# Optimization experiments

Hardware: AMD Instinct MI355X
Metric: run time of the kernel (lower is better)

Reference implementation:

```python
import jax, jax.numpy as jnp
import numpy as np

D_MODEL = 1024
D_STATE = 16
EXPAND = 2
D_INNER = EXPAND * D_MODEL
BATCH = 8
SEQ = 2048


def _linear_init(key, fan_in, shape):
    bound = 1.0 / np.sqrt(fan_in)
    return jax.random.uniform(key, shape, jnp.float32, -bound, bound)


def setup_inputs() -> dict:
    key = jax.random.key(0)
    ks = jax.random.split(key, 9)
    x = jax.random.normal(ks[0], (BATCH, SEQ, D_MODEL), jnp.float32)
    W_in = _linear_init(ks[1], D_MODEL, (D_MODEL, 2 * D_INNER))
    b_in = _linear_init(ks[2], D_MODEL, (2 * D_INNER,))
    W_x = _linear_init(ks[3], D_INNER, (D_INNER, 2 * D_STATE))
    b_x = _linear_init(ks[4], D_INNER, (2 * D_STATE,))
    W_dt = _linear_init(ks[5], D_INNER, (D_INNER, D_INNER))
    b_dt = _linear_init(ks[6], D_INNER, (D_INNER,))
    W_out = _linear_init(ks[7], D_INNER, (D_INNER, D_MODEL))
    b_out = _linear_init(ks[8], D_INNER, (D_MODEL,))
    # A_log = log(arange(1, d_state+1)) tiled over d_inner rows
    A = jnp.tile(jnp.arange(1, D_STATE + 1, dtype=jnp.float32), (D_INNER, 1))
    A_log = jnp.log(A)
    D_param = jnp.ones((D_INNER,), jnp.float32)
    return dict(x=x, W_in=W_in, b_in=b_in, W_x=W_x, b_x=b_x, W_dt=W_dt,
                b_dt=b_dt, W_out=W_out, b_out=b_out, A_log=A_log, D_param=D_param)


def _silu(v):
    return v * jax.nn.sigmoid(v)


def reference(x, W_in, b_in, W_x, b_x, W_dt, b_dt, W_out, b_out, A_log, D_param):
    # in_proj -> split into x branch and gate z
    xz = x @ W_in + b_in                      # [B,S,2*d_inner]
    x_proj, z = jnp.split(xz, 2, axis=-1)
    u = _silu(x_proj)                          # x_conv (no conv branch)
    A = -jnp.exp(A_log)                        # [d_inner, d_state]
    x_dbl = u @ W_x + b_x                      # [B,S,2*d_state]
    Bm, Cm = jnp.split(x_dbl, 2, axis=-1)      # each [B,S,d_state]
    dt = jax.nn.softplus(u @ W_dt + b_dt)      # [B,S,d_inner]

    # selective scan: recurrence over time via lax.scan
    uT = jnp.swapaxes(u, 0, 1)                 # [S,B,d_inner]
    dtT = jnp.swapaxes(dt, 0, 1)
    BT = jnp.swapaxes(Bm, 0, 1)                # [S,B,d_state]
    CT = jnp.swapaxes(Cm, 0, 1)

    def step(h, inp):
        u_t, dt_t, B_t, C_t = inp
        dA = jnp.exp(dt_t[..., None] * A)                       # [B,d_inner,d_state]
        h = h * dA + (dt_t * u_t)[..., None] * B_t[:, None, :]  # [B,d_inner,d_state]
        y_t = jnp.einsum('bds,bs->bd', h, C_t) + D_param * u_t  # [B,d_inner]
        return h, y_t

    h0 = jnp.zeros((x.shape[0], D_INNER, D_STATE), x.dtype)
    _, yT = jax.lax.scan(step, h0, (uT, dtT, BT, CT))
    y = jnp.swapaxes(yT, 0, 1)                 # [B,S,d_inner]
    y = y * _silu(z)
    return y @ W_out + b_out                   # [B,S,d_model]
```

## Files before the change

kernel.cpp:

```cpp
#include <hip/hip_runtime.h>
#include <hip/hip_bf16.h>

typedef __hip_bfloat16 bf16;
typedef short v8s __attribute__((ext_vector_type(8)));
typedef float v4f __attribute__((ext_vector_type(4)));

#define DMODEL 1024
#define DINNER 2048
#define NSTATE 16
#define NBATCH 8
#define SEQLEN 2048
#define MROWS  (NBATCH*SEQLEN)
#define NCHUNK 32
#define CHLEN  (SEQLEN/NCHUNK)

#define SBAR() do { __builtin_amdgcn_sched_barrier(0); \
                    __builtin_amdgcn_s_barrier(); \
                    __builtin_amdgcn_sched_barrier(0); } while(0)

__device__ __forceinline__ float b2f(bf16 x){ return __bfloat162float(x); }
__device__ __forceinline__ bf16  f2b(float x){ return __float2bfloat16(x); }

__device__ __forceinline__ void gload_lds16(const bf16* g, bf16* l){
  __builtin_amdgcn_global_load_lds((const __attribute__((address_space(1))) void*)g,
                                   (__attribute__((address_space(3))) void*)l, 16, 0, 0);
}

__global__ __launch_bounds__(256) void cvt_f32_bf16(const float* __restrict__ src,
                                                    bf16* __restrict__ dst, int n4){
  const int gid = blockIdx.x*256 + threadIdx.x;
  if (gid >= n4) return;
  const float4 v = ((const float4*)src)[gid];
  union { bf16 h[4]; short4 s; } u;
  u.h[0] = f2b(v.x); u.h[1] = f2b(v.y); u.h[2] = f2b(v.z); u.h[3] = f2b(v.w);
  ((short4*)dst)[gid] = u.s;
}

__global__ __launch_bounds__(256) void transpose64(const float* __restrict__ src,
                                                   bf16* __restrict__ dst, int K, int N){
  __shared__ bf16 t[64][65];
  const int n0 = blockIdx.x*64, k0 = blockIdx.y*64;
  const int tx = threadIdx.x & 63, ty = threadIdx.x >> 6;
  for (int r = ty; r < 64; r += 4)
    t[r][tx] = f2b(src[(size_t)(k0+r)*N + n0+tx]);
  __syncthreads();
  for (int r = ty; r < 64; r += 4)
    dst[(size_t)(n0+r)*K + k0+tx] = t[tx][r];
}

__global__ __launch_bounds__(256) void padT_wx(const float* __restrict__ wx, bf16* __restrict__ wxt){
  const int gid = blockIdx.x*256 + threadIdx.x;
  const int n = gid >> 11, k = gid & 2047;
  wxt[gid] = (n < 32) ? f2b(wx[(size_t)k*32 + n]) : f2b(0.f);
}

__global__ __launch_bounds__(256) void prep_aneg(const float* __restrict__ alog, float* __restrict__ an){
  const int gid = blockIdx.x*256 + threadIdx.x;
  an[gid] = -__expf(alog[gid]);
}

template<int EPI>
__global__ __launch_bounds__(512, 2) void gemm256(
    const bf16* __restrict__ A, int lda,
    const bf16* __restrict__ Bt,
    const float* __restrict__ bias,
    void* __restrict__ Out, int ldc, int K, int nbx)
{
  extern __shared__ __align__(16) bf16 lds[];
  const int tid = threadIdx.x;
  const int lane = tid & 63, w = tid >> 6;
  const int wm = w >> 2, wn = w & 3;
  const int lr = lane & 15, lk = lane >> 4;

  const int nwg = gridDim.x;
  const int swz = (blockIdx.x & 7) * (nwg >> 3) + (blockIdx.x >> 3);
  const int nby = nwg / nbx;
  const int bx = swz / nby, by = swz % nby;
  const int m0 = by*256, n0 = bx*256;

  const int idx0 = w*64 + lane, idx1 = 512 + idx0;
  const int r0 = idx0 >> 3, r1 = idx1 >> 3;
  const int c0 = ((idx0 & 7) ^ (r0 & 7)) * 8, c1 = ((idx1 & 7) ^ (r1 & 7)) * 8;
  const size_t offA0 = (size_t)r0*lda + c0, offA1 = (size_t)r1*lda + c1;
  const size_t offB0 = (size_t)r0*K   + c0, offB1 = (size_t)r1*K   + c1;
  const int ld0 = w*512, ld1 = 4096 + w*512;

  const bf16* Abase = A  + (size_t)m0*lda;
  const bf16* Bbase = Bt + (size_t)n0*K;

  const int kb0 = (lk*16)      ^ ((lr & 7) << 4);
  const int kb1 = (64 + lk*16) ^ ((lr & 7) << 4);
  const int arow = (wm*128 + lr) * 128;
  const int brow = (wn*64  + lr) * 128;

  v4f acc[8][4];
#pragma unroll
  for (int i=0;i<8;i++)
#pragma unroll
    for (int j=0;j<4;j++) acc[i][j] = (v4f){0.f,0.f,0.f,0.f};

  auto stageTile = [&](int t){
    const bf16* ga = Abase + (size_t)t*64;
    const bf16* gbp = Bbase + (size_t)t*64;
    bf16* la = lds + (t&1)*32768;
    bf16* lb = la + 16384;
    gload_lds16(ga + offA0,                     la + ld0);
    gload_lds16(ga + offA1,                     la + ld1);
    gload_lds16(ga + offA0 + (size_t)128*lda,   la + 8192 + ld0);
    gload_lds16(ga + offA1 + (size_t)128*lda,   la + 8192 + ld1);
    gload_lds16(gbp + offB0,                    lb + ld0);
    gload_lds16(gbp + offB1,                    lb + ld1);
    gload_lds16(gbp + offB0 + (size_t)128*K,    lb + 8192 + ld0);
    gload_lds16(gbp + offB1 + (size_t)128*K,    lb + 8192 + ld1);
  };

  const int nt = K >> 6;
  stageTile(0);

  for (int t=0; t<nt; ++t){
    const char* Ab = (const char*)(lds + (t&1)*32768);
    const char* Bb = Ab + 32768;

    asm volatile("s_waitcnt vmcnt(0)" ::: "memory");
    SBAR();
    if (t+1 < nt) stageTile(t+1);

    __builtin_amdgcn_s_setprio(1);
    v8s bfr[4][2];
#pragma unroll
    for (int j=0;j<4;j++){
      bfr[j][0] = *(const v8s*)(Bb + brow + j*2048 + kb0);
      bfr[j][1] = *(const v8s*)(Bb + brow + j*2048 + kb1);
    }
#pragma unroll
    for (int q=0;q<4;q++){
      v8s aq[2][2];
#pragma unroll
      for (int i=0;i<2;i++){
        aq[i][0] = *(const v8s*)(Ab + arow + (q*2+i)*2048 + kb0);
        aq[i][1] = *(const v8s*)(Ab + arow + (q*2+i)*2048 + kb1);
      }
#pragma unroll
      for (int i=0;i<2;i++)
#pragma unroll
        for (int j=0;j<4;j++){
          acc[q*2+i][j] = __builtin_amdgcn_mfma_f32_16x16x32_bf16(aq[i][0], bfr[j][0], acc[q*2+i][j], 0,0,0);
          acc[q*2+i][j] = __builtin_amdgcn_mfma_f32_16x16x32_bf16(aq[i][1], bfr[j][1], acc[q*2+i][j], 0,0,0);
        }
    }
    __builtin_amdgcn_s_setprio(0);
  }

  float bv[4];
#pragma unroll
  for (int j=0;j<4;j++) bv[j] = bias[n0 + wn*64 + j*16 + lr];
#pragma unroll
  for (int rb=0; rb<8; rb++){
    const int gmb = m0 + wm*128 + rb*16 + lk*4;
#pragma unroll
    for (int j=0;j<4;j++){
      const int gn = n0 + wn*64 + j*16 + lr;
#pragma unroll
      for (int r=0;r<4;r++){
        float v = acc[rb][j][r] + bv[j];
        if (EPI == 0){
          v = v / (1.f + __expf(-v));
          ((bf16*)Out)[(size_t)(gmb+r)*ldc + gn] = f2b(v);
        } else if (EPI == 1){
          v = fmaxf(v, 0.f) + log1pf(__expf(-fabsf(v)));
          ((bf16*)Out)[(size_t)(gmb+r)*ldc + gn] = f2b(v);
        } else {
          ((float*)Out)[(size_t)(gmb+r)*ldc + gn] = v;
        }
      }
    }
  }
}

template<int EPI>
__global__ __launch_bounds__(256) void gemm_bt(
    const bf16* __restrict__ A, int lda,
    const bf16* __restrict__ Bt,
    const float* __restrict__ bias,
    void* __restrict__ Out, int ldc, int K)
{
  __shared__ __align__(16) bf16 Asm[2][128*64];
  __shared__ __align__(16) bf16 Bsm[2][128*64];
  const int tid = threadIdx.x;
  const int m0 = blockIdx.y*128, n0 = blockIdx.x*128;
  const int lane = tid & 63, wid = tid >> 6;
  const int wm = wid >> 1, wn = wid & 1;
  const int lr = lane & 15, lk = lane >> 4;

  v4f acc[4][4];
#pragma unroll
  for (int i=0;i<4;i++)
#pragma unroll
    for (int j=0;j<4;j++) acc[i][j] = (v4f){0.f,0.f,0.f,0.f};

  size_t aoff[4], boff[4]; int soff[4];
#pragma unroll
  for (int i=0;i<4;i++){
    const int idx = i*256 + tid;
    const int r = idx >> 3, c8 = idx & 7;
    const int c8s = c8 ^ (r & 7);
    aoff[i] = (size_t)r*lda + c8s*8;
    boff[i] = (size_t)r*K   + c8s*8;
    soff[i] = (i*256 + wid*64)*8;
  }
  const bf16* Abase = A  + (size_t)m0*lda;
  const bf16* Bbase = Bt + (size_t)n0*K;

  auto compute = [&](int buf){
#pragma unroll
    for (int kk=0;kk<2;kk++){
      v8s af[4], bfr[4];
#pragma unroll
      for (int mi=0;mi<4;mi++){
        const int row = wm*64 + mi*16 + lr;
        const int kb = (kk*64 + lk*16) ^ ((row & 7) << 4);
        af[mi] = *(const v8s*)((const char*)&Asm[buf][0] + row*128 + kb);
      }
#pragma unroll
      for (int ni=0;ni<4;ni++){
        const int row = wn*64 + ni*16 + lr;
        const int kb = (kk*64 + lk*16) ^ ((row & 7) << 4);
        bfr[ni] = *(const v8s*)((const char*)&Bsm[buf][0] + row*128 + kb);
      }
#pragma unroll
      for (int mi=0;mi<4;mi++)
#pragma unroll
        for (int ni=0;ni<4;ni++)
          acc[mi][ni] = __builtin_amdgcn_mfma_f32_16x16x32_bf16(af[mi], bfr[ni], acc[mi][ni], 0, 0, 0);
    }
  };

  const int nt = K >> 6;
#pragma unroll
  for (int i=0;i<4;i++){
    gload_lds16(Abase + aoff[i], &Asm[0][soff[i]]);
    gload_lds16(Bbase + boff[i], &Bsm[0][soff[i]]);
  }
  int cur = 0;
  for (int t=0; t<nt-1; ++t){
    __syncthreads();
    const bf16* An = Abase + (size_t)(t+1)*64;
    const bf16* Bn = Bbase + (size_t)(t+1)*64;
#pragma unroll
    for (int i=0;i<4;i++){
      gload_lds16(An + aoff[i], &Asm[cur^1][soff[i]]);
      gload_lds16(Bn + boff[i], &Bsm[cur^1][soff[i]]);
    }
    compute(cur);
    cur ^= 1;
  }
  __syncthreads();
  compute(cur);

#pragma unroll
  for (int mi=0;mi<4;mi++){
#pragma unroll
    for (int ni=0;ni<4;ni++){
      const int gn = n0 + wn*64 + ni*16 + lr;
      float bb = (gn < 32) ? bias[gn] : 0.f;
#pragma unroll
      for (int r=0;r<4;r++){
        const int gm = m0 + wm*64 + mi*16 + lk*4 + r;
        float v = acc[mi][ni][r] + bb;
        if (gn < 32) ((float*)Out)[(size_t)gm*32 + gn] = v;
      }
    }
  }
}

__global__ __launch_bounds__(256) void scan_passA(
    const bf16* __restrict__ xz, const bf16* __restrict__ dtb,
    const float* __restrict__ bc, const float* __restrict__ an,
    float* __restrict__ hC, float* __restrict__ sD)
{
  const int bx = blockIdx.x;
  const int d = (bx & 7)*256 + threadIdx.x;
  const int b = (bx >> 3) & 7;
  const int c = bx >> 6;
  float a[16], h[16];
#pragma unroll
  for (int j=0;j<16;j++){ a[j] = an[d*16+j]; h[j] = 0.f; }
  float sdt = 0.f;
  const int m0 = b*SEQLEN + c*CHLEN;
  for (int s=0;s<CHLEN;++s){
    const size_t m = (size_t)(m0 + s);
    const float uf  = b2f(xz[m*4096 + d]);
    const float dtf = b2f(dtb[m*2048 + d]);
    const float du = dtf*uf;
    sdt += dtf;
    const float4* bp = (const float4*)&bc[m*32];
    const float4 B0=bp[0],B1=bp[1],B2=bp[2],B3=bp[3];
    const float Bv[16] = {B0.x,B0.y,B0.z,B0.w,B1.x,B1.y,B1.z,B1.w,
                          B2.x,B2.y,B2.z,B2.w,B3.x,B3.y,B3.z,B3.w};
#pragma unroll
    for (int j=0;j<16;j++)
      h[j] = h[j]*__expf(dtf*a[j]) + du*Bv[j];
  }
  const size_t off = ((size_t)(c*8 + b)*2048 + d);
  float4* hp = (float4*)&hC[off*16];
  hp[0] = make_float4(h[0],h[1],h[2],h[3]);
  hp[1] = make_float4(h[4],h[5],h[6],h[7]);
  hp[2] = make_float4(h[8],h[9],h[10],h[11]);
  hp[3] = make_float4(h[12],h[13],h[14],h[15]);
  sD[off] = sdt;
}

__global__ __launch_bounds__(256) void scan_passB(
    const float* __restrict__ an, float* __restrict__ hC, const float* __restrict__ sD)
{
  const int gid = blockIdx.x*256 + threadIdx.x;
  const int d = gid & 2047, b = gid >> 11;
  float a[16], h0[16];
#pragma unroll
  for (int j=0;j<16;j++){ a[j] = an[d*16+j]; h0[j] = 0.f; }
  for (int c=0;c<NCHUNK;c++){
    const size_t off = ((size_t)(c*8 + b)*2048 + d);
    float4* hp = (float4*)&hC[off*16];
    const float4 t0=hp[0], t1=hp[1], t2=hp[2], t3=hp[3];
    const float sdt = sD[off];
    const float ht[16] = {t0.x,t0.y,t0.z,t0.w,t1.x,t1.y,t1.z,t1.w,
                          t2.x,t2.y,t2.z,t2.w,t3.x,t3.y,t3.z,t3.w};
    hp[0] = make_float4(h0[0],h0[1],h0[2],h0[3]);
    hp[1] = make_float4(h0[4],h0[5],h0[6],h0[7]);
    hp[2] = make_float4(h0[8],h0[9],h0[10],h0[11]);
    hp[3] = make_float4(h0[12],h0[13],h0[14],h0[15]);
#pragma unroll
    for (int j=0;j<16;j++)
      h0[j] = ht[j] + __expf(sdt*a[j])*h0[j];
  }
}

__global__ __launch_bounds__(256) void scan_passC(
    bf16* __restrict__ xz, const bf16* __restrict__ dtb,
    const float* __restrict__ bc, const float* __restrict__ an,
    const float* __restrict__ hC, const float* __restrict__ Dp)
{
  const int bx = blockIdx.x;
  const int d = (bx & 7)*256 + threadIdx.x;
  const int b = (bx >> 3) & 7;
  const int c = bx >> 6;
  float a[16], h[16];
#pragma unroll
  for (int j=0;j<16;j++) a[j] = an[d*16+j];
  {
    const size_t off = ((size_t)(c*8 + b)*2048 + d);
    const float4* hp = (const float4*)&hC[off*16];
    const float4 t0=hp[0], t1=hp[1], t2=hp[2], t3=hp[3];
    h[0]=t0.x;h[1]=t0.y;h[2]=t0.z;h[3]=t0.w; h[4]=t1.x;h[5]=t1.y;h[6]=t1.z;h[7]=t1.w;
    h[8]=t2.x;h[9]=t2.y;h[10]=t2.z;h[11]=t2.w; h[12]=t3.x;h[13]=t3.y;h[14]=t3.z;h[15]=t3.w;
  }
  const float dpar = Dp[d];
  const int m0 = b*SEQLEN + c*CHLEN;
  for (int s=0;s<CHLEN;++s){
    const size_t m = (size_t)(m0 + s);
    const float uf  = b2f(xz[m*4096 + d]);
    const float szf = b2f(xz[m*4096 + 2048 + d]);
    const float dtf = b2f(dtb[m*2048 + d]);
    const float du = dtf*uf;
    const float4* bp = (const float4*)&bc[m*32];
    const float4 B0=bp[0],B1=bp[1],B2=bp[2],B3=bp[3];
    const float4 C0=bp[4],C1=bp[5],C2=bp[6],C3=bp[7];
    const float Bv[16] = {B0.x,B0.y,B0.z,B0.w,B1.x,B1.y,B1.z,B1.w,
                          B2.x,B2.y,B2.z,B2.w,B3.x,B3.y,B3.z,B3.w};
    const float Cv[16] = {C0.x,C0.y,C0.z,C0.w,C1.x,C1.y,C1.z,C1.w,
                          C2.x,C2.y,C2.z,C2.w,C3.x,C3.y,C3.z,C3.w};
    float y = 0.f;
#pragma unroll
    for (int j=0;j<16;j++){
      h[j] = h[j]*__expf(dtf*a[j]) + du*Bv[j];
      y += h[j]*Cv[j];
    }
    y = (y + dpar*uf) * szf;
    xz[m*4096 + d] = f2b(y);
  }
}

extern "C" void kernel_launch(void* const* d_in, const int* in_sizes, int n_in,
                              void* d_out, int out_size, void* d_ws, size_t ws_size,
                              hipStream_t stream) {
  const float* x      = (const float*)d_in[0];
  const float* W_in   = (const float*)d_in[1];
  const float* b_in   = (const float*)d_in[2];
  const float* W_x    = (const float*)d_in[3];
  const float* b_x    = (const float*)d_in[4];
  const float* W_dt   = (const float*)d_in[5];
  const float* b_dt   = (const float*)d_in[6];
  const float* W_out  = (const float*)d_in[7];
  const float* b_out  = (const float*)d_in[8];
  const float* A_log  = (const float*)d_in[9];
  const float* D_par  = (const float*)d_in[10];
  float* out = (float*)d_out;

  char* ws = (char*)d_ws;
  size_t off = 0;
  auto alloc = [&](size_t bytes)->void*{ void* p = ws + off; off += (bytes + 255) & ~(size_t)255; return p; };
  bf16*  WinT  = (bf16*) alloc((size_t)4096*1024*2);
  bf16*  WdtT  = (bf16*) alloc((size_t)2048*2048*2);
  bf16*  WoutT = (bf16*) alloc((size_t)1024*2048*2);
  bf16*  WxT   = (bf16*) alloc((size_t)128*2048*2);
  bf16*  xz    = (bf16*) alloc((size_t)MROWS*4096*2);
  bf16*  dtb   = (bf16*) alloc((size_t)MROWS*2048*2);
  float* bc    = (float*)alloc((size_t)MROWS*32*4);
  float* an    = (float*)alloc((size_t)2048*16*4);
  float* sD    = (float*)alloc((size_t)NCHUNK*MROWS*4);
  float* hC    = (float*)d_out;
  bf16*  xb    = dtb;
  (void)in_sizes; (void)n_in; (void)out_size; (void)ws_size;

  hipFuncSetAttribute((const void*)gemm256<0>, hipFuncAttributeMaxDynamicSharedMemorySize, 131072);
  hipFuncSetAttribute((const void*)gemm256<1>, hipFuncAttributeMaxDynamicSharedMemorySize, 131072);
  hipFuncSetAttribute((const void*)gemm256<2>, hipFuncAttributeMaxDynamicSharedMemorySize, 131072);

  cvt_f32_bf16<<<(MROWS*1024/4 + 255)/256, 256, 0, stream>>>(x, xb, MROWS*1024/4);
  transpose64<<<dim3(4096/64, 1024/64), 256, 0, stream>>>(W_in,  WinT,  1024, 4096);
  transpose64<<<dim3(2048/64, 2048/64), 256, 0, stream>>>(W_dt,  WdtT,  2048, 2048);
  transpose64<<<dim3(1024/64, 2048/64), 256, 0, stream>>>(W_out, WoutT, 2048, 1024);
  padT_wx<<<1024, 256, 0, stream>>>(W_x, WxT);
  prep_aneg<<<128, 256, 0, stream>>>(A_log, an);

  gemm256<0><<<1024, 512, 131072, stream>>>(xb, 1024, WinT, b_in, xz, 4096, 1024, 16);
  gemm256<1><<<512, 512, 131072, stream>>>(xz, 4096, WdtT, b_dt, dtb, 2048, 2048, 8);
  gemm_bt<3><<<dim3(1, MROWS/128), 256, 0, stream>>>(xz, 4096, WxT, b_x, bc, 32, 2048);
  scan_passA<<<8*8*NCHUNK, 256, 0, stream>>>(xz, dtb, bc, an, hC, sD);
  scan_passB<<<MROWS/256, 256, 0, stream>>>(an, hC, sD);
  scan_passC<<<8*8*NCHUNK, 256, 0, stream>>>(xz, dtb, bc, an, hC, D_par);
  gemm256<2><<<256, 512, 131072, stream>>>(xz, 4096, WoutT, b_out, out, 1024, 2048, 4);
}
```

Measured before the change: 735.7 us.

## Shrink GEMM tile to 256x128 with K=32 steps and static LDS

Restructures the bf16 MFMA GEMM from a 256x256 tile with K-step 64 and 128KB dynamic LDS to a 256x128 tile with K-step 32, using 48KB of static double-buffered LDS. The wave layout becomes 4x2 waves, each holding a 64x64 accumulator, and the launch bound rises to 4 blocks per CU. Grids double for all three projection GEMMs. The intent is higher occupancy and more blocks, so that latency hiding and load balance improve. The cost is lower arithmetic intensity per loaded byte and twice as many barriers per unit of K.

```diff
diff --git a/kernel.cpp b/kernel.cpp
--- a/kernel.cpp
+++ b/kernel.cpp
@@ -60,94 +60,75 @@
 }
 
 template<int EPI>
-__global__ __launch_bounds__(512, 2) void gemm256(
+__global__ __launch_bounds__(512, 4) void gemm256(
     const bf16* __restrict__ A, int lda,
     const bf16* __restrict__ Bt,
     const float* __restrict__ bias,
     void* __restrict__ Out, int ldc, int K, int nbx)
 {
-  extern __shared__ __align__(16) bf16 lds[];
+  __shared__ __align__(16) bf16 lds[2*12288];
   const int tid = threadIdx.x;
   const int lane = tid & 63, w = tid >> 6;
-  const int wm = w >> 2, wn = w & 3;
+  const int wm = w >> 1, wn = w & 1;
   const int lr = lane & 15, lk = lane >> 4;
 
   const int nwg = gridDim.x;
   const int swz = (blockIdx.x & 7) * (nwg >> 3) + (blockIdx.x >> 3);
   const int nby = nwg / nbx;
   const int bx = swz / nby, by = swz % nby;
-  const int m0 = by*256, n0 = bx*256;
-
-  const int idx0 = w*64 + lane, idx1 = 512 + idx0;
-  const int r0 = idx0 >> 3, r1 = idx1 >> 3;
-  const int c0 = ((idx0 & 7) ^ (r0 & 7)) * 8, c1 = ((idx1 & 7) ^ (r1 & 7)) * 8;
-  const size_t offA0 = (size_t)r0*lda + c0, offA1 = (size_t)r1*lda + c1;
-  const size_t offB0 = (size_t)r0*K   + c0, offB1 = (size_t)r1*K   + c1;
-  const int ld0 = w*512, ld1 = 4096 + w*512;
+  const int m0 = by*256, n0 = bx*128;
+
+  const int ar = tid >> 2, asl = (tid & 3) ^ (ar & 3);
+  const size_t aoff0 = (size_t)ar*lda + asl*8;
+  const size_t aoff1 = aoff0 + (size_t)128*lda;
+  const size_t boff0 = (size_t)ar*K + asl*8;
+  const int ldA0 = __builtin_amdgcn_readfirstlane(w*512);
+  const int ldA1 = __builtin_amdgcn_readfirstlane(4096 + w*512);
+  const int ldB0 = __builtin_amdgcn_readfirstlane(8192 + w*512);
 
   const bf16* Abase = A  + (size_t)m0*lda;
   const bf16* Bbase = Bt + (size_t)n0*K;
 
-  const int kb0 = (lk*16)      ^ ((lr & 7) << 4);
-  const int kb1 = (64 + lk*16) ^ ((lr & 7) << 4);
-  const int arow = (wm*128 + lr) * 128;
-  const int brow = (wn*64  + lr) * 128;
-
-  v4f acc[8][4];
-#pragma unroll
-  for (int i=0;i<8;i++)
+  const int kb = ((lk ^ (lr & 3)) << 4);
+  const int arow = wm*4096 + lr*64;
+  const int brow = 16384 + wn*4096 + lr*64;
+
+  v4f acc[4][4];
+#pragma unroll
+  for (int i=0;i<4;i++)
 #pragma unroll
     for (int j=0;j<4;j++) acc[i][j] = (v4f){0.f,0.f,0.f,0.f};
 
   auto stageTile = [&](int t){
-    const bf16* ga = Abase + (size_t)t*64;
-    const bf16* gbp = Bbase + (size_t)t*64;
-    bf16* la = lds + (t&1)*32768;
-    bf16* lb = la + 16384;
-    gload_lds16(ga + offA0,                     la + ld0);
-    gload_lds16(ga + offA1,                     la + ld1);
-    gload_lds16(ga + offA0 + (size_t)128*lda,   la + 8192 + ld0);
-    gload_lds16(ga + offA1 + (size_t)128*lda,   la + 8192 + ld1);
-    gload_lds16(gbp + offB0,                    lb + ld0);
-    gload_lds16(gbp + offB1,                    lb + ld1);
-    gload_lds16(gbp + offB0 + (size_t)128*K,    lb + 8192 + ld0);
-    gload_lds16(gbp + offB1 + (size_t)128*K,    lb + 8192 + ld1);
+    const bf16* ga = Abase + (size_t)t*32;
+    const bf16* gb = Bbase + (size_t)t*32;
+    bf16* l = lds + (t&1)*12288;
+    gload_lds16(ga + aoff0, l + ldA0);
+    gload_lds16(ga + aoff1, l + ldA1);
+    gload_lds16(gb + boff0, l + ldB0);
   };
 
-  const int nt = K >> 6;
+  const int nt = K >> 5;
   stageTile(0);
 
   for (int t=0; t<nt; ++t){
-    const char* Ab = (const char*)(lds + (t&1)*32768);
-    const char* Bb = Ab + 32768;
+    const char* Lb = (const char*)lds + (t&1)*24576;
 
     asm volatile("s_waitcnt vmcnt(0)" ::: "memory");
     SBAR();
     if (t+1 < nt) stageTile(t+1);
 
     __builtin_amdgcn_s_setprio(1);
-    v8s bfr[4][2];
-#pragma unroll
-    for (int j=0;j<4;j++){
-      bfr[j][0] = *(const v8s*)(Bb + brow + j*2048 + kb0);
-      bfr[j][1] = *(const v8s*)(Bb + brow + j*2048 + kb1);
-    }
-#pragma unroll
-    for (int q=0;q<4;q++){
-      v8s aq[2][2];
-#pragma unroll
-      for (int i=0;i<2;i++){
-        aq[i][0] = *(const v8s*)(Ab + arow + (q*2+i)*2048 + kb0);
-        aq[i][1] = *(const v8s*)(Ab + arow + (q*2+i)*2048 + kb1);
-      }
-#pragma unroll
-      for (int i=0;i<2;i++)
-#pragma unroll
-        for (int j=0;j<4;j++){
-          acc[q*2+i][j] = __builtin_amdgcn_mfma_f32_16x16x32_bf16(aq[i][0], bfr[j][0], acc[q*2+i][j], 0,0,0);
-          acc[q*2+i][j] = __builtin_amdgcn_mfma_f32_16x16x32_bf16(aq[i][1], bfr[j][1], acc[q*2+i][j], 0,0,0);
-        }
-    }
+    v8s a[4], b[4];
+#pragma unroll
+    for (int ni=0;ni<4;ni++) b[ni] = *(const v8s*)(Lb + brow + ni*1024 + kb);
+#pragma unroll
+    for (int mi=0;mi<4;mi++) a[mi] = *(const v8s*)(Lb + arow + mi*1024 + kb);
+#pragma unroll
+    for (int mi=0;mi<4;mi++)
+#pragma unroll
+      for (int ni=0;ni<4;ni++)
+        acc[mi][ni] = __builtin_amdgcn_mfma_f32_16x16x32_bf16(a[mi], b[ni], acc[mi][ni], 0,0,0);
     __builtin_amdgcn_s_setprio(0);
   }
 
@@ -155,14 +136,14 @@
 #pragma unroll
   for (int j=0;j<4;j++) bv[j] = bias[n0 + wn*64 + j*16 + lr];
 #pragma unroll
-  for (int rb=0; rb<8; rb++){
-    const int gmb = m0 + wm*128 + rb*16 + lk*4;
-#pragma unroll
-    for (int j=0;j<4;j++){
-      const int gn = n0 + wn*64 + j*16 + lr;
+  for (int mi=0;mi<4;mi++){
+    const int gmb = m0 + wm*64 + mi*16 + lk*4;
+#pragma unroll
+    for (int ni=0;ni<4;ni++){
+      const int gn = n0 + wn*64 + ni*16 + lr;
 #pragma unroll
       for (int r=0;r<4;r++){
-        float v = acc[rb][j][r] + bv[j];
+        float v = acc[mi][ni][r] + bv[ni];
         if (EPI == 0){
           v = v / (1.f + __expf(-v));
           ((bf16*)Out)[(size_t)(gmb+r)*ldc + gn] = f2b(v);
@@ -412,10 +393,6 @@
   bf16*  xb    = dtb;
   (void)in_sizes; (void)n_in; (void)out_size; (void)ws_size;
 
-  hipFuncSetAttribute((const void*)gemm256<0>, hipFuncAttributeMaxDynamicSharedMemorySize, 131072);
-  hipFuncSetAttribute((const void*)gemm256<1>, hipFuncAttributeMaxDynamicSharedMemorySize, 131072);
-  hipFuncSetAttribute((const void*)gemm256<2>, hipFuncAttributeMaxDynamicSharedMemorySize, 131072);
-
   cvt_f32_bf16<<<(MROWS*1024/4 + 255)/256, 256, 0, stream>>>(x, xb, MROWS*1024/4);
   transpose64<<<dim3(4096/64, 1024/64), 256, 0, stream>>>(W_in,  WinT,  1024, 4096);
   transpose64<<<dim3(2048/64, 2048/64), 256, 0, stream>>>(W_dt,  WdtT,  2048, 2048);
@@ -423,11 +400,11 @@
   padT_wx<<<1024, 256, 0, stream>>>(W_x, WxT);
   prep_aneg<<<128, 256, 0, stream>>>(A_log, an);
 
-  gemm256<0><<<1024, 512, 131072, stream>>>(xb, 1024, WinT, b_in, xz, 4096, 1024, 16);
-  gemm256<1><<<512, 512, 131072, stream>>>(xz, 4096, WdtT, b_dt, dtb, 2048, 2048, 8);
+  gemm256<0><<<2048, 512, 0, stream>>>(xb, 1024, WinT, b_in, xz, 4096, 1024, 32);
+  gemm256<1><<<1024, 512, 0, stream>>>(xz, 4096, WdtT, b_dt, dtb, 2048, 2048, 16);
   gemm_bt<3><<<dim3(1, MROWS/128), 256, 0, stream>>>(xz, 4096, WxT, b_x, bc, 32, 2048);
   scan_passA<<<8*8*NCHUNK, 256, 0, stream>>>(xz, dtb, bc, an, hC, sD);
   scan_passB<<<MROWS/256, 256, 0, stream>>>(an, hC, sD);
   scan_passC<<<8*8*NCHUNK, 256, 0, stream>>>(xz, dtb, bc, an, hC, D_par);
-  gemm256<2><<<256, 512, 131072, stream>>>(xz, 4096, WoutT, b_out, out, 1024, 2048, 4);
-}
+  gemm256<2><<<512, 512, 0, stream>>>(xz, 4096, WoutT, b_out, out, 1024, 2048, 8);
+}
```

After: 899.1 us. 22.2% more time.

## Split GEMM K-tile into 32-wide slabs with interleaved async staging

Applied to the files above, without the earlier changes.

The 256x256 bf16 GEMM's 64-wide K tile is split into two 32-wide k-slabs, each with its own A and B LDS regions and a new 64-byte-row XOR swizzle. Next-tile global-to-LDS loads are issued one slab at a time between MFMA phases. Partial vmcnt waits replace the full drain, and there are two barriers per tile. The aim is to overlap memory traffic with MFMA work and cut stall time at the barrier. The cost is an extra barrier per tile and more complex wait-count bookkeeping.

```diff
diff --git a/kernel.cpp b/kernel.cpp
--- a/kernel.cpp
+++ b/kernel.cpp
@@ -78,20 +78,34 @@
   const int bx = swz / nby, by = swz % nby;
   const int m0 = by*256, n0 = bx*256;
 
-  const int idx0 = w*64 + lane, idx1 = 512 + idx0;
-  const int r0 = idx0 >> 3, r1 = idx1 >> 3;
-  const int c0 = ((idx0 & 7) ^ (r0 & 7)) * 8, c1 = ((idx1 & 7) ^ (r1 & 7)) * 8;
-  const size_t offA0 = (size_t)r0*lda + c0, offA1 = (size_t)r1*lda + c1;
-  const size_t offB0 = (size_t)r0*K   + c0, offB1 = (size_t)r1*K   + c1;
-  const int ld0 = w*512, ld1 = 4096 + w*512;
-
   const bf16* Abase = A  + (size_t)m0*lda;
   const bf16* Bbase = Bt + (size_t)n0*K;
 
-  const int kb0 = (lk*16)      ^ ((lr & 7) << 4);
-  const int kb1 = (64 + lk*16) ^ ((lr & 7) << 4);
-  const int arow = (wm*128 + lr) * 128;
-  const int brow = (wn*64  + lr) * 128;
+  const int srow = tid >> 2;
+  const int ssl  = (tid & 3) ^ ((tid >> 3) & 3);
+  const size_t aoff0 = (size_t)srow*lda + ssl*8;
+  const size_t aoff1 = aoff0 + (size_t)128*lda;
+  const size_t boff0 = (size_t)srow*K   + ssl*8;
+  const size_t boff1 = boff0 + (size_t)128*K;
+  const int ldst = w*512;
+
+  auto stageSlab = [&](int t, int s){
+    const int ks = s >> 1;
+    bf16* dst = lds + (t&1)*32768 + (s&1)*16384 + ks*8192;
+    if (!(s&1)){
+      const bf16* g = Abase + (size_t)(t*64 + ks*32);
+      gload_lds16(g + aoff0, dst + ldst);
+      gload_lds16(g + aoff1, dst + 4096 + ldst);
+    } else {
+      const bf16* g = Bbase + (size_t)(t*64 + ks*32);
+      gload_lds16(g + boff0, dst + ldst);
+      gload_lds16(g + boff1, dst + 4096 + ldst);
+    }
+  };
+
+  const int kbR  = ((lk ^ ((lr >> 1) & 3)) << 4);
+  const int arowB = (wm*128 + lr)*64 + kbR;
+  const int browB = (wn*64  + lr)*64 + kbR;
 
   v4f acc[8][4];
 #pragma unroll
@@ -99,55 +113,74 @@
 #pragma unroll
     for (int j=0;j<4;j++) acc[i][j] = (v4f){0.f,0.f,0.f,0.f};
 
-  auto stageTile = [&](int t){
-    const bf16* ga = Abase + (size_t)t*64;
-    const bf16* gbp = Bbase + (size_t)t*64;
-    bf16* la = lds + (t&1)*32768;
-    bf16* lb = la + 16384;
-    gload_lds16(ga + offA0,                     la + ld0);
-    gload_lds16(ga + offA1,                     la + ld1);
-    gload_lds16(ga + offA0 + (size_t)128*lda,   la + 8192 + ld0);
-    gload_lds16(ga + offA1 + (size_t)128*lda,   la + 8192 + ld1);
-    gload_lds16(gbp + offB0,                    lb + ld0);
-    gload_lds16(gbp + offB1,                    lb + ld1);
-    gload_lds16(gbp + offB0 + (size_t)128*K,    lb + 8192 + ld0);
-    gload_lds16(gbp + offB1 + (size_t)128*K,    lb + 8192 + ld1);
-  };
-
   const int nt = K >> 6;
-  stageTile(0);
+  stageSlab(0,0); stageSlab(0,1); stageSlab(0,2); stageSlab(0,3);
 
   for (int t=0; t<nt; ++t){
-    const char* Ab = (const char*)(lds + (t&1)*32768);
-    const char* Bb = Ab + 32768;
-
-    asm volatile("s_waitcnt vmcnt(0)" ::: "memory");
+    const char* db = (const char*)lds + (t&1)*65536;
+    const bool more = (t+1) < nt;
+    v8s bfr[4], af[4];
+
+    if (more){
+      stageSlab(t+1, 0);
+      __builtin_amdgcn_sched_barrier(0);
+      asm volatile("s_waitcnt vmcnt(6)" ::: "memory");
+    } else {
+      asm volatile("s_waitcnt vmcnt(4)" ::: "memory");
+    }
     SBAR();
-    if (t+1 < nt) stageTile(t+1);
-
+#pragma unroll
+    for (int cf=0;cf<4;cf++) bfr[cf] = *(const v8s*)(db + 32768 + browB + cf*1024);
+#pragma unroll
+    for (int rf=0;rf<4;rf++) af[rf] = *(const v8s*)(db + arowB + rf*1024);
     __builtin_amdgcn_s_setprio(1);
-    v8s bfr[4][2];
-#pragma unroll
-    for (int j=0;j<4;j++){
-      bfr[j][0] = *(const v8s*)(Bb + brow + j*2048 + kb0);
-      bfr[j][1] = *(const v8s*)(Bb + brow + j*2048 + kb1);
-    }
-#pragma unroll
-    for (int q=0;q<4;q++){
-      v8s aq[2][2];
-#pragma unroll
-      for (int i=0;i<2;i++){
-        aq[i][0] = *(const v8s*)(Ab + arow + (q*2+i)*2048 + kb0);
-        aq[i][1] = *(const v8s*)(Ab + arow + (q*2+i)*2048 + kb1);
-      }
-#pragma unroll
-      for (int i=0;i<2;i++)
-#pragma unroll
-        for (int j=0;j<4;j++){
-          acc[q*2+i][j] = __builtin_amdgcn_mfma_f32_16x16x32_bf16(aq[i][0], bfr[j][0], acc[q*2+i][j], 0,0,0);
-          acc[q*2+i][j] = __builtin_amdgcn_mfma_f32_16x16x32_bf16(aq[i][1], bfr[j][1], acc[q*2+i][j], 0,0,0);
-        }
-    }
+#pragma unroll
+    for (int rf=0;rf<4;rf++)
+#pragma unroll
+      for (int cf=0;cf<4;cf++)
+        acc[rf][cf] = __builtin_amdgcn_mfma_f32_16x16x32_bf16(af[rf], bfr[cf], acc[rf][cf], 0,0,0);
+    __builtin_amdgcn_s_setprio(0);
+
+    if (more) stageSlab(t+1, 1);
+#pragma unroll
+    for (int rf=0;rf<4;rf++) af[rf] = *(const v8s*)(db + arowB + 4096 + rf*1024);
+    __builtin_amdgcn_s_setprio(1);
+#pragma unroll
+    for (int rf=0;rf<4;rf++)
+#pragma unroll
+      for (int cf=0;cf<4;cf++)
+        acc[4+rf][cf] = __builtin_amdgcn_mfma_f32_16x16x32_bf16(af[rf], bfr[cf], acc[4+rf][cf], 0,0,0);
+    __builtin_amdgcn_s_setprio(0);
+
+    if (more){
+      stageSlab(t+1, 2);
+      __builtin_amdgcn_sched_barrier(0);
+      asm volatile("s_waitcnt vmcnt(6)" ::: "memory");
+    } else {
+      asm volatile("s_waitcnt vmcnt(0)" ::: "memory");
+    }
+    SBAR();
+#pragma unroll
+    for (int cf=0;cf<4;cf++) bfr[cf] = *(const v8s*)(db + 32768 + 16384 + browB + cf*1024);
+#pragma unroll
+    for (int rf=0;rf<4;rf++) af[rf] = *(const v8s*)(db + 16384 + arowB + rf*1024);
+    __builtin_amdgcn_s_setprio(1);
+#pragma unroll
+    for (int rf=0;rf<4;rf++)
+#pragma unroll
+      for (int cf=0;cf<4;cf++)
+        acc[rf][cf] = __builtin_amdgcn_mfma_f32_16x16x32_bf16(af[rf], bfr[cf], acc[rf][cf], 0,0,0);
+    __builtin_amdgcn_s_setprio(0);
+
+    if (more) stageSlab(t+1, 3);
+#pragma unroll
+    for (int rf=0;rf<4;rf++) af[rf] = *(const v8s*)(db + 16384 + arowB + 4096 + rf*1024);
+    __builtin_amdgcn_s_setprio(1);
+#pragma unroll
+    for (int rf=0;rf<4;rf++)
+#pragma unroll
+      for (int cf=0;cf<4;cf++)
+        acc[4+rf][cf] = __builtin_amdgcn_mfma_f32_16x16x32_bf16(af[rf], bfr[cf], acc[4+rf][cf], 0,0,0);
     __builtin_amdgcn_s_setprio(0);
   }
 
```

New measurement: 766.1 us. 1.04x slower.
